# Optimization experiments

Hardware: AMD Instinct MI355X
Metric: run time of the kernel (lower is better)

The kernel has to match this reference:

```python
import jax, jax.numpy as jnp
import numpy as np

N = 100000       # nodes
E = 3200000      # edges (avg degree 32)
IN_F = 256
OUT_F = 128


def setup_inputs() -> dict:
    key = jax.random.key(0)
    k1, k2, k3, k4, k5, k6 = jax.random.split(key, 6)
    x = jax.random.normal(k1, (N, IN_F), dtype=jnp.float32)
    adj_row = jax.random.randint(k2, (E,), 0, N, dtype=jnp.int64)
    adj_col = jax.random.randint(k3, (E,), 0, N, dtype=jnp.int64)
    adj_val = jax.random.uniform(k4, (E,), dtype=jnp.float32)
    stdv = 1.0 / np.sqrt(OUT_F)
    weight = jax.random.uniform(k5, (IN_F, OUT_F), dtype=jnp.float32, minval=-stdv, maxval=stdv)
    bias = jax.random.uniform(k6, (OUT_F,), dtype=jnp.float32, minval=-stdv, maxval=stdv)
    return {"x": x, "adj_row": adj_row, "adj_col": adj_col,
            "adj_val": adj_val, "weight": weight, "bias": bias}


def reference(x, adj_row, adj_col, adj_val, weight, bias):
    # dropout with p=0 is identity
    support = x @ weight                                   # [N, OUT_F] dense GEMM
    # spmm(adj, support): gather neighbor rows, scale by edge value, segment-sum into rows
    gathered = adj_val[:, None] * support[adj_col]         # [E, OUT_F]
    out = jax.ops.segment_sum(gathered, adj_row, num_segments=N)  # [N, OUT_F]
    return jax.nn.relu(out + bias)
```

## Files before the change

kernel.cpp:

```cpp
#include <hip/hip_runtime.h>

#define N_NODES 100000
#define IN_F 256
#define OUT_F 128
#define RPB 64
#define RSHIFT 6
#define NB 1563
#define CAPG 2560
#define CHUNK_SC 4096

typedef short bf16x8 __attribute__((ext_vector_type(8)));
typedef float f32x4  __attribute__((ext_vector_type(4)));

static __device__ __forceinline__ unsigned short f2bf(float f) {
    unsigned int u = __float_as_uint(f);
    u = (u + 0x7FFF + ((u >> 16) & 1)) >> 16;
    return (unsigned short)u;
}

__global__ __launch_bounds__(256) void wt_kernel(const float* __restrict__ w,
                                                 unsigned short* __restrict__ wT,
                                                 int* __restrict__ gcur) {
    int n = blockIdx.x;
    int k = threadIdx.x;
    wT[n * IN_F + k] = f2bf(w[(size_t)k * OUT_F + n]);
    if (blockIdx.x < 7) {
        int i = blockIdx.x * 256 + threadIdx.x;
        if (i < NB) gcur[i] = i * CAPG;
    }
}

__global__ __launch_bounds__(256) void gemm_mfma_kernel(const float* __restrict__ x,
                                                        const unsigned short* __restrict__ wT,
                                                        unsigned short* __restrict__ supb) {
    __shared__ unsigned short A_lds[32][264];

    const int tid  = threadIdx.x;
    const int wave = tid >> 6;
    const int lane = tid & 63;
    const int quad = lane >> 4;
    const int l15  = lane & 15;
    const int row_base = blockIdx.x * 32;

    bf16x8 bfrag[2][8];
    {
        const unsigned short* wb = wT + (size_t)(wave * 32 + l15) * IN_F + quad * 8;
#pragma unroll
        for (int ct = 0; ct < 2; ++ct)
#pragma unroll
            for (int ks = 0; ks < 8; ++ks)
                bfrag[ct][ks] = *(const bf16x8*)(wb + ct * 16 * IN_F + ks * 32);
    }

    {
        const float* xb = x + (size_t)row_base * IN_F;
#pragma unroll
        for (int i = 0; i < 8; ++i) {
            int fidx = i * 1024 + tid * 4;
            float4 a = *(const float4*)(xb + fidx);
            int r = fidx >> 8;
            int c = fidx & 255;
            ushort4 u = {f2bf(a.x), f2bf(a.y), f2bf(a.z), f2bf(a.w)};
            *(ushort4*)&A_lds[r][c] = u;
        }
    }
    __syncthreads();

    f32x4 acc[2][2];
#pragma unroll
    for (int rt = 0; rt < 2; ++rt)
#pragma unroll
        for (int ct = 0; ct < 2; ++ct) acc[rt][ct] = (f32x4){0.f, 0.f, 0.f, 0.f};

#pragma unroll
    for (int ks = 0; ks < 8; ++ks) {
        bf16x8 a0 = *(const bf16x8*)&A_lds[l15][ks * 32 + quad * 8];
        bf16x8 a1 = *(const bf16x8*)&A_lds[16 + l15][ks * 32 + quad * 8];
        acc[0][0] = __builtin_amdgcn_mfma_f32_16x16x32_bf16(a0, bfrag[0][ks], acc[0][0], 0, 0, 0);
        acc[0][1] = __builtin_amdgcn_mfma_f32_16x16x32_bf16(a0, bfrag[1][ks], acc[0][1], 0, 0, 0);
        acc[1][0] = __builtin_amdgcn_mfma_f32_16x16x32_bf16(a1, bfrag[0][ks], acc[1][0], 0, 0, 0);
        acc[1][1] = __builtin_amdgcn_mfma_f32_16x16x32_bf16(a1, bfrag[1][ks], acc[1][1], 0, 0, 0);
    }

#pragma unroll
    for (int rt = 0; rt < 2; ++rt)
#pragma unroll
        for (int ct = 0; ct < 2; ++ct)
#pragma unroll
            for (int r = 0; r < 4; ++r) {
                int orow = row_base + rt * 16 + quad * 4 + r;
                int ocol = wave * 32 + ct * 16 + l15;
                supb[(size_t)orow * OUT_F + ocol] = f2bf(acc[rt][ct][r]);
            }
}

__global__ __launch_bounds__(256) void scatter_kernel(const int* __restrict__ adj_row,
                                                      const int* __restrict__ adj_col,
                                                      const float* __restrict__ adj_val,
                                                      int* __restrict__ gcur,
                                                      int2* __restrict__ ebuf, int E) {
    __shared__ int pref[NB + 1];
    __shared__ int shf[NB];
    __shared__ int2 se[CHUNK_SC];
    __shared__ int wsum[4];

    const int tid  = threadIdx.x;
    const int base = blockIdx.x * CHUNK_SC;
    const int m    = min(CHUNK_SC, E - base);
    const int nv   = m >> 2;

    for (int b = tid; b <= NB; b += 256) pref[b] = 0;
    __syncthreads();

    for (int j = tid; j < nv; j += 256) {
        int4 r4 = ((const int4*)(adj_row + base))[j];
        atomicAdd(&pref[r4.x >> RSHIFT], 1);
        atomicAdd(&pref[r4.y >> RSHIFT], 1);
        atomicAdd(&pref[r4.z >> RSHIFT], 1);
        atomicAdd(&pref[r4.w >> RSHIFT], 1);
    }
    if (tid < (m & 3)) atomicAdd(&pref[adj_row[base + (nv << 2) + tid] >> RSHIFT], 1);
    __syncthreads();

    {
        int loc[7];
        const int bb = tid * 7;
        int s = 0;
#pragma unroll
        for (int g = 0; g < 7; ++g) {
            int b = bb + g;
            int v = (b < NB) ? pref[b] : 0;
            loc[g] = s;
            s += v;
        }
        const int lane = tid & 63, wv = tid >> 6;
        int inc = s;
        for (int d = 1; d < 64; d <<= 1) {
            int t = __shfl_up(inc, d, 64);
            if (lane >= d) inc += t;
        }
        if (lane == 63) wsum[wv] = inc;
        __syncthreads();
        int wb2 = 0;
        for (int k = 0; k < wv; ++k) wb2 += wsum[k];
        const int texcl = wb2 + inc - s;
#pragma unroll
        for (int g = 0; g < 7; ++g) {
            int b = bb + g;
            if (b < NB) pref[b] = texcl + loc[g];
        }
        if (tid == 255) pref[NB] = texcl + s;
    }
    __syncthreads();

    for (int b = tid; b < NB; b += 256) {
        int s0 = pref[b];
        int c  = pref[b + 1] - s0;
        if (c > 0) shf[b] = atomicAdd(&gcur[b], c) - s0;
    }
    __syncthreads();

    for (int j = tid; j < nv; j += 256) {
        int4   c4 = ((const int4*)(adj_col + base))[j];
        int4   r4 = ((const int4*)(adj_row + base))[j];
        float4 v4 = ((const float4*)(adj_val + base))[j];
        int p;
        p = atomicAdd(&pref[r4.x >> RSHIFT], 1);
        se[p] = make_int2(c4.x | ((r4.x & (RPB - 1)) << 17), __float_as_int(v4.x));
        p = atomicAdd(&pref[r4.y >> RSHIFT], 1);
        se[p] = make_int2(c4.y | ((r4.y & (RPB - 1)) << 17), __float_as_int(v4.y));
        p = atomicAdd(&pref[r4.z >> RSHIFT], 1);
        se[p] = make_int2(c4.z | ((r4.z & (RPB - 1)) << 17), __float_as_int(v4.z));
        p = atomicAdd(&pref[r4.w >> RSHIFT], 1);
        se[p] = make_int2(c4.w | ((r4.w & (RPB - 1)) << 17), __float_as_int(v4.w));
    }
    if (tid < (m & 3)) {
        int i = base + (nv << 2) + tid;
        int r = adj_row[i];
        int p = atomicAdd(&pref[r >> RSHIFT], 1);
        se[p] = make_int2(adj_col[i] | ((r & (RPB - 1)) << 17), __float_as_int(adj_val[i]));
    }
    __syncthreads();

    for (int p = tid; p < m; p += 256) {
        int lo = 0, hi = NB - 1;
        while (lo < hi) {
            int mid = (lo + hi) >> 1;
            if (pref[mid] > p) hi = mid; else lo = mid + 1;
        }
        int g = shf[lo] + p;
        if (g < (lo + 1) * CAPG) ebuf[g] = se[p];
    }
}

__global__ __launch_bounds__(512) void spmm_kernel(const int2* __restrict__ ebuf,
                                                   const int* __restrict__ gcur,
                                                   const unsigned short* __restrict__ supb,
                                                   const float* __restrict__ bias,
                                                   float* __restrict__ out) {
    __shared__ int2 se[CAPG];
    __shared__ int cnt[RPB];
    __shared__ int off[RPB];
    __shared__ int cur[RPB];

    const int tid  = threadIdx.x;
    const int b    = blockIdx.x;
    const int wave = tid >> 6;
    const int lane = tid & 63;
    const int f0   = lane * 2;

    const int start = b * CAPG;
    int m = gcur[b] - start;
    if (m > CAPG) m = CAPG;

    if (tid < RPB) cnt[tid] = 0;
    __syncthreads();

    int2 ev[5];
#pragma unroll
    for (int j = 0; j < 5; ++j) {
        int i = j * 512 + tid;
        if (i < m) {
            ev[j] = ebuf[start + i];
            atomicAdd(&cnt[ev[j].x >> 17], 1);
        }
    }
    __syncthreads();

    if (tid < RPB) {
        int v = cnt[tid];
        int s = v;
#pragma unroll
        for (int d = 1; d < RPB; d <<= 1) {
            int t = __shfl_up(s, d, 64);
            if (tid >= d) s += t;
        }
        off[tid] = s - v;
        cur[tid] = s - v;
    }
    __syncthreads();

#pragma unroll
    for (int j = 0; j < 5; ++j) {
        int i = j * 512 + tid;
        if (i < m) {
            int p = atomicAdd(&cur[ev[j].x >> 17], 1);
            se[p] = ev[j];
        }
    }
    __syncthreads();

    float2 acc[8];
#pragma unroll
    for (int j = 0; j < 8; ++j) acc[j] = make_float2(0.f, 0.f);

#pragma unroll
    for (int j = 0; j < 8; ++j) {
        int r = wave * 8 + j;
        int o = off[r];
        int c = cnt[r];
        float2 a = acc[j];
        int i = 0;
        for (; i + 4 <= c; i += 4) {
            int2 e0 = se[o + i + 0];
            int2 e1 = se[o + i + 1];
            int2 e2 = se[o + i + 2];
            int2 e3 = se[o + i + 3];
            unsigned int u0 = *(const unsigned int*)(supb + (size_t)(e0.x & 0x1FFFF) * OUT_F + f0);
            unsigned int u1 = *(const unsigned int*)(supb + (size_t)(e1.x & 0x1FFFF) * OUT_F + f0);
            unsigned int u2 = *(const unsigned int*)(supb + (size_t)(e2.x & 0x1FFFF) * OUT_F + f0);
            unsigned int u3 = *(const unsigned int*)(supb + (size_t)(e3.x & 0x1FFFF) * OUT_F + f0);
            float v0 = __int_as_float(e0.y), v1 = __int_as_float(e1.y);
            float v2 = __int_as_float(e2.y), v3 = __int_as_float(e3.y);
            a.x += v0 * __uint_as_float(u0 << 16);
            a.y += v0 * __uint_as_float(u0 & 0xFFFF0000u);
            a.x += v1 * __uint_as_float(u1 << 16);
            a.y += v1 * __uint_as_float(u1 & 0xFFFF0000u);
            a.x += v2 * __uint_as_float(u2 << 16);
            a.y += v2 * __uint_as_float(u2 & 0xFFFF0000u);
            a.x += v3 * __uint_as_float(u3 << 16);
            a.y += v3 * __uint_as_float(u3 & 0xFFFF0000u);
        }
        for (; i < c; ++i) {
            int2 e = se[o + i];
            unsigned int u = *(const unsigned int*)(supb + (size_t)(e.x & 0x1FFFF) * OUT_F + f0);
            float v = __int_as_float(e.y);
            a.x += v * __uint_as_float(u << 16);
            a.y += v * __uint_as_float(u & 0xFFFF0000u);
        }
        acc[j] = a;
    }

    float2 bv = *((const float2*)bias + lane);
    const int rbase = b << RSHIFT;
#pragma unroll
    for (int j = 0; j < 8; ++j) {
        int grow = rbase + wave * 8 + j;
        if (grow < N_NODES) {
            float2 o;
            o.x = fmaxf(acc[j].x + bv.x, 0.f);
            o.y = fmaxf(acc[j].y + bv.y, 0.f);
            *((float2*)(out + (size_t)grow * OUT_F) + lane) = o;
        }
    }
}

extern "C" void kernel_launch(void* const* d_in, const int* in_sizes, int n_in,
                              void* d_out, int out_size, void* d_ws, size_t ws_size,
                              hipStream_t stream) {
    const float* x       = (const float*)d_in[0];
    const int*   adj_row = (const int*)d_in[1];
    const int*   adj_col = (const int*)d_in[2];
    const float* adj_val = (const float*)d_in[3];
    const float* weight  = (const float*)d_in[4];
    const float* bias    = (const float*)d_in[5];
    float* out = (float*)d_out;
    const int E = in_sizes[1];

    char* p = (char*)d_ws;
    unsigned short* supb = (unsigned short*)p;  p += (size_t)N_NODES * OUT_F * 2;
    int2* ebuf           = (int2*)p;            p += (size_t)NB * CAPG * 8;
    unsigned short* wT   = (unsigned short*)p;  p += (size_t)OUT_F * IN_F * 2;
    int* gcur            = (int*)p;             p += (size_t)NB * 4;

    wt_kernel<<<OUT_F, 256, 0, stream>>>(weight, wT, gcur);
    gemm_mfma_kernel<<<N_NODES / 32, 256, 0, stream>>>(x, wT, supb);
    scatter_kernel<<<(E + CHUNK_SC - 1) / CHUNK_SC, 256, 0, stream>>>(adj_row, adj_col,
                                                                      adj_val, gcur, ebuf, E);
    spmm_kernel<<<NB, 512, 0, stream>>>(ebuf, gcur, supb, bias, out);
}
```

Baseline: 372.0 us.

## Replace bucketed LDS edge sort with global per-row CSR built via atomics

Drops the two-level bucketed scatter (per-chunk LDS sort into fixed-capacity 64-row groups, then a per-block LDS re-sort in spmm). Instead it builds an exact CSR: row degree histogram fused into the GEMM kernel with global atomics, a three-kernel prefix scan, a global-atomic scatter into per-row slots, and an spmm that reads each row's edges straight from global memory. This removes the LDS re-sort and the capacity-truncation risk. In exchange it adds millions of contended global atomics, uncoalesced scattered 8-byte writes, and three extra kernel launches plus a memset.

```diff
diff --git a/kernel.cpp b/kernel.cpp
--- a/kernel.cpp
+++ b/kernel.cpp
@@ -3,11 +3,7 @@
 #define N_NODES 100000
 #define IN_F 256
 #define OUT_F 128
-#define RPB 64
-#define RSHIFT 6
-#define NB 1563
-#define CAPG 2560
-#define CHUNK_SC 4096
+#define ROWS_PER_SBLK 391
 
 typedef short bf16x8 __attribute__((ext_vector_type(8)));
 typedef float f32x4  __attribute__((ext_vector_type(4)));
@@ -19,20 +15,17 @@
 }
 
 __global__ __launch_bounds__(256) void wt_kernel(const float* __restrict__ w,
-                                                 unsigned short* __restrict__ wT,
-                                                 int* __restrict__ gcur) {
+                                                 unsigned short* __restrict__ wT) {
     int n = blockIdx.x;
     int k = threadIdx.x;
     wT[n * IN_F + k] = f2bf(w[(size_t)k * OUT_F + n]);
-    if (blockIdx.x < 7) {
-        int i = blockIdx.x * 256 + threadIdx.x;
-        if (i < NB) gcur[i] = i * CAPG;
-    }
 }
 
 __global__ __launch_bounds__(256) void gemm_mfma_kernel(const float* __restrict__ x,
                                                         const unsigned short* __restrict__ wT,
-                                                        unsigned short* __restrict__ supb) {
+                                                        unsigned short* __restrict__ supb,
+                                                        const int* __restrict__ adj_row,
+                                                        int* __restrict__ rowcnt, int E) {
     __shared__ unsigned short A_lds[32][264];
 
     const int tid  = threadIdx.x;
@@ -41,6 +34,19 @@
     const int quad = lane >> 4;
     const int l15  = lane & 15;
     const int row_base = blockIdx.x * 32;
+
+    {
+        const int nv4 = E >> 2;
+        for (int i = blockIdx.x * 256 + tid; i < nv4; i += 3125 * 256) {
+            int4 r4 = ((const int4*)adj_row)[i];
+            atomicAdd(&rowcnt[r4.x], 1);
+            atomicAdd(&rowcnt[r4.y], 1);
+            atomicAdd(&rowcnt[r4.z], 1);
+            atomicAdd(&rowcnt[r4.w], 1);
+        }
+        if (blockIdx.x == 0 && tid < (E & 3))
+            atomicAdd(&rowcnt[adj_row[(nv4 << 2) + tid]], 1);
+    }
 
     bf16x8 bfrag[2][8];
     {
@@ -94,182 +100,124 @@
             }
 }
 
+__global__ __launch_bounds__(256) void scan1_kernel(const int* __restrict__ rowcnt,
+                                                    int* __restrict__ bsum) {
+    __shared__ int ws[4];
+    const int g = blockIdx.x, tid = threadIdx.x;
+    const int base = g * ROWS_PER_SBLK;
+    int s = 0;
+    for (int i = tid; i < ROWS_PER_SBLK; i += 256) {
+        int r = base + i;
+        if (r < N_NODES) s += rowcnt[r];
+    }
+#pragma unroll
+    for (int d = 1; d < 64; d <<= 1) s += __shfl_xor(s, d, 64);
+    if ((tid & 63) == 0) ws[tid >> 6] = s;
+    __syncthreads();
+    if (tid == 0) bsum[g] = ws[0] + ws[1] + ws[2] + ws[3];
+}
+
+__global__ __launch_bounds__(256) void scan2_kernel(const int* __restrict__ bsum,
+                                                    int* __restrict__ bbase) {
+    __shared__ int ws[4];
+    const int tid = threadIdx.x;
+    const int lane = tid & 63, wv = tid >> 6;
+    int v = bsum[tid];
+    int inc = v;
+#pragma unroll
+    for (int d = 1; d < 64; d <<= 1) {
+        int t = __shfl_up(inc, d, 64);
+        if (lane >= d) inc += t;
+    }
+    if (lane == 63) ws[wv] = inc;
+    __syncthreads();
+    int wb = 0;
+    for (int k = 0; k < wv; ++k) wb += ws[k];
+    bbase[tid] = wb + inc - v;
+}
+
+__global__ __launch_bounds__(256) void scan3_kernel(const int* __restrict__ rowcnt,
+                                                    const int* __restrict__ bbase,
+                                                    int* __restrict__ rowoff,
+                                                    int* __restrict__ rowcur) {
+    __shared__ int ws[4];
+    const int g = blockIdx.x, tid = threadIdx.x;
+    const int base = g * ROWS_PER_SBLK;
+    const int r0 = base + 2 * tid, r1 = r0 + 1;
+    const bool ok0 = (2 * tid < ROWS_PER_SBLK) && (r0 < N_NODES);
+    const bool ok1 = (2 * tid + 1 < ROWS_PER_SBLK) && (r1 < N_NODES);
+    int a = ok0 ? rowcnt[r0] : 0;
+    int b = ok1 ? rowcnt[r1] : 0;
+    int s = a + b;
+    const int lane = tid & 63, wv = tid >> 6;
+    int inc = s;
+#pragma unroll
+    for (int d = 1; d < 64; d <<= 1) {
+        int t = __shfl_up(inc, d, 64);
+        if (lane >= d) inc += t;
+    }
+    if (lane == 63) ws[wv] = inc;
+    __syncthreads();
+    int wb = 0;
+    for (int k = 0; k < wv; ++k) wb += ws[k];
+    const int excl = bbase[g] + wb + inc - s;
+    if (ok0) { rowoff[r0] = excl;     rowcur[r0] = excl; }
+    if (ok1) { rowoff[r1] = excl + a; rowcur[r1] = excl + a; }
+}
+
 __global__ __launch_bounds__(256) void scatter_kernel(const int* __restrict__ adj_row,
                                                       const int* __restrict__ adj_col,
                                                       const float* __restrict__ adj_val,
-                                                      int* __restrict__ gcur,
+                                                      int* __restrict__ rowcur,
                                                       int2* __restrict__ ebuf, int E) {
-    __shared__ int pref[NB + 1];
-    __shared__ int shf[NB];
-    __shared__ int2 se[CHUNK_SC];
-    __shared__ int wsum[4];
-
-    const int tid  = threadIdx.x;
-    const int base = blockIdx.x * CHUNK_SC;
-    const int m    = min(CHUNK_SC, E - base);
-    const int nv   = m >> 2;
-
-    for (int b = tid; b <= NB; b += 256) pref[b] = 0;
-    __syncthreads();
-
-    for (int j = tid; j < nv; j += 256) {
-        int4 r4 = ((const int4*)(adj_row + base))[j];
-        atomicAdd(&pref[r4.x >> RSHIFT], 1);
-        atomicAdd(&pref[r4.y >> RSHIFT], 1);
-        atomicAdd(&pref[r4.z >> RSHIFT], 1);
-        atomicAdd(&pref[r4.w >> RSHIFT], 1);
-    }
-    if (tid < (m & 3)) atomicAdd(&pref[adj_row[base + (nv << 2) + tid] >> RSHIFT], 1);
-    __syncthreads();
-
-    {
-        int loc[7];
-        const int bb = tid * 7;
-        int s = 0;
-#pragma unroll
-        for (int g = 0; g < 7; ++g) {
-            int b = bb + g;
-            int v = (b < NB) ? pref[b] : 0;
-            loc[g] = s;
-            s += v;
-        }
-        const int lane = tid & 63, wv = tid >> 6;
-        int inc = s;
-        for (int d = 1; d < 64; d <<= 1) {
-            int t = __shfl_up(inc, d, 64);
-            if (lane >= d) inc += t;
-        }
-        if (lane == 63) wsum[wv] = inc;
-        __syncthreads();
-        int wb2 = 0;
-        for (int k = 0; k < wv; ++k) wb2 += wsum[k];
-        const int texcl = wb2 + inc - s;
-#pragma unroll
-        for (int g = 0; g < 7; ++g) {
-            int b = bb + g;
-            if (b < NB) pref[b] = texcl + loc[g];
-        }
-        if (tid == 255) pref[NB] = texcl + s;
-    }
-    __syncthreads();
-
-    for (int b = tid; b < NB; b += 256) {
-        int s0 = pref[b];
-        int c  = pref[b + 1] - s0;
-        if (c > 0) shf[b] = atomicAdd(&gcur[b], c) - s0;
-    }
-    __syncthreads();
-
-    for (int j = tid; j < nv; j += 256) {
-        int4   c4 = ((const int4*)(adj_col + base))[j];
-        int4   r4 = ((const int4*)(adj_row + base))[j];
-        float4 v4 = ((const float4*)(adj_val + base))[j];
+    const int gid = blockIdx.x * 256 + threadIdx.x;
+    const int nv4 = E >> 2;
+    for (int j = gid; j < nv4; j += gridDim.x * 256) {
+        int4   r4 = ((const int4*)adj_row)[j];
+        int4   c4 = ((const int4*)adj_col)[j];
+        float4 v4 = ((const float4*)adj_val)[j];
         int p;
-        p = atomicAdd(&pref[r4.x >> RSHIFT], 1);
-        se[p] = make_int2(c4.x | ((r4.x & (RPB - 1)) << 17), __float_as_int(v4.x));
-        p = atomicAdd(&pref[r4.y >> RSHIFT], 1);
-        se[p] = make_int2(c4.y | ((r4.y & (RPB - 1)) << 17), __float_as_int(v4.y));
-        p = atomicAdd(&pref[r4.z >> RSHIFT], 1);
-        se[p] = make_int2(c4.z | ((r4.z & (RPB - 1)) << 17), __float_as_int(v4.z));
-        p = atomicAdd(&pref[r4.w >> RSHIFT], 1);
-        se[p] = make_int2(c4.w | ((r4.w & (RPB - 1)) << 17), __float_as_int(v4.w));
-    }
-    if (tid < (m & 3)) {
-        int i = base + (nv << 2) + tid;
-        int r = adj_row[i];
-        int p = atomicAdd(&pref[r >> RSHIFT], 1);
-        se[p] = make_int2(adj_col[i] | ((r & (RPB - 1)) << 17), __float_as_int(adj_val[i]));
-    }
-    __syncthreads();
-
-    for (int p = tid; p < m; p += 256) {
-        int lo = 0, hi = NB - 1;
-        while (lo < hi) {
-            int mid = (lo + hi) >> 1;
-            if (pref[mid] > p) hi = mid; else lo = mid + 1;
-        }
-        int g = shf[lo] + p;
-        if (g < (lo + 1) * CAPG) ebuf[g] = se[p];
-    }
-}
-
-__global__ __launch_bounds__(512) void spmm_kernel(const int2* __restrict__ ebuf,
-                                                   const int* __restrict__ gcur,
+        p = atomicAdd(&rowcur[r4.x], 1); ebuf[p] = make_int2(c4.x, __float_as_int(v4.x));
+        p = atomicAdd(&rowcur[r4.y], 1); ebuf[p] = make_int2(c4.y, __float_as_int(v4.y));
+        p = atomicAdd(&rowcur[r4.z], 1); ebuf[p] = make_int2(c4.z, __float_as_int(v4.z));
+        p = atomicAdd(&rowcur[r4.w], 1); ebuf[p] = make_int2(c4.w, __float_as_int(v4.w));
+    }
+    if (gid < (E & 3)) {
+        int i = (nv4 << 2) + gid;
+        int p = atomicAdd(&rowcur[adj_row[i]], 1);
+        ebuf[p] = make_int2(adj_col[i], __float_as_int(adj_val[i]));
+    }
+}
+
+__global__ __launch_bounds__(256) void spmm_kernel(const int2* __restrict__ ebuf,
+                                                   const int* __restrict__ rowoff,
+                                                   const int* __restrict__ rowend,
                                                    const unsigned short* __restrict__ supb,
                                                    const float* __restrict__ bias,
                                                    float* __restrict__ out) {
-    __shared__ int2 se[CAPG];
-    __shared__ int cnt[RPB];
-    __shared__ int off[RPB];
-    __shared__ int cur[RPB];
-
     const int tid  = threadIdx.x;
-    const int b    = blockIdx.x;
-    const int wave = tid >> 6;
+    const int wave = __builtin_amdgcn_readfirstlane(tid >> 6);
     const int lane = tid & 63;
     const int f0   = lane * 2;
-
-    const int start = b * CAPG;
-    int m = gcur[b] - start;
-    if (m > CAPG) m = CAPG;
-
-    if (tid < RPB) cnt[tid] = 0;
-    __syncthreads();
-
-    int2 ev[5];
-#pragma unroll
-    for (int j = 0; j < 5; ++j) {
-        int i = j * 512 + tid;
-        if (i < m) {
-            ev[j] = ebuf[start + i];
-            atomicAdd(&cnt[ev[j].x >> 17], 1);
-        }
-    }
-    __syncthreads();
-
-    if (tid < RPB) {
-        int v = cnt[tid];
-        int s = v;
-#pragma unroll
-        for (int d = 1; d < RPB; d <<= 1) {
-            int t = __shfl_up(s, d, 64);
-            if (tid >= d) s += t;
-        }
-        off[tid] = s - v;
-        cur[tid] = s - v;
-    }
-    __syncthreads();
-
-#pragma unroll
-    for (int j = 0; j < 5; ++j) {
-        int i = j * 512 + tid;
-        if (i < m) {
-            int p = atomicAdd(&cur[ev[j].x >> 17], 1);
-            se[p] = ev[j];
-        }
-    }
-    __syncthreads();
-
-    float2 acc[8];
-#pragma unroll
-    for (int j = 0; j < 8; ++j) acc[j] = make_float2(0.f, 0.f);
-
-#pragma unroll
+    const int rbase = blockIdx.x * 32 + wave * 8;
+    const float2 bv = *((const float2*)bias + lane);
+
     for (int j = 0; j < 8; ++j) {
-        int r = wave * 8 + j;
-        int o = off[r];
-        int c = cnt[r];
-        float2 a = acc[j];
+        const int r = rbase + j;
+        const int o = rowoff[r];
+        const int c = rowend[r] - o;
+        const int2* ep = ebuf + o;
+        float2 a = make_float2(0.f, 0.f);
         int i = 0;
         for (; i + 4 <= c; i += 4) {
-            int2 e0 = se[o + i + 0];
-            int2 e1 = se[o + i + 1];
-            int2 e2 = se[o + i + 2];
-            int2 e3 = se[o + i + 3];
-            unsigned int u0 = *(const unsigned int*)(supb + (size_t)(e0.x & 0x1FFFF) * OUT_F + f0);
-            unsigned int u1 = *(const unsigned int*)(supb + (size_t)(e1.x & 0x1FFFF) * OUT_F + f0);
-            unsigned int u2 = *(const unsigned int*)(supb + (size_t)(e2.x & 0x1FFFF) * OUT_F + f0);
-            unsigned int u3 = *(const unsigned int*)(supb + (size_t)(e3.x & 0x1FFFF) * OUT_F + f0);
+            int2 e0 = ep[i + 0];
+            int2 e1 = ep[i + 1];
+            int2 e2 = ep[i + 2];
+            int2 e3 = ep[i + 3];
+            unsigned int u0 = *(const unsigned int*)(supb + (size_t)e0.x * OUT_F + f0);
+            unsigned int u1 = *(const unsigned int*)(supb + (size_t)e1.x * OUT_F + f0);
+            unsigned int u2 = *(const unsigned int*)(supb + (size_t)e2.x * OUT_F + f0);
+            unsigned int u3 = *(const unsigned int*)(supb + (size_t)e3.x * OUT_F + f0);
             float v0 = __int_as_float(e0.y), v1 = __int_as_float(e1.y);
             float v2 = __int_as_float(e2.y), v3 = __int_as_float(e3.y);
             a.x += v0 * __uint_as_float(u0 << 16);
@@ -282,26 +230,16 @@
             a.y += v3 * __uint_as_float(u3 & 0xFFFF0000u);
         }
         for (; i < c; ++i) {
-            int2 e = se[o + i];
-            unsigned int u = *(const unsigned int*)(supb + (size_t)(e.x & 0x1FFFF) * OUT_F + f0);
+            int2 e = ep[i];
+            unsigned int u = *(const unsigned int*)(supb + (size_t)e.x * OUT_F + f0);
             float v = __int_as_float(e.y);
             a.x += v * __uint_as_float(u << 16);
             a.y += v * __uint_as_float(u & 0xFFFF0000u);
         }
-        acc[j] = a;
-    }
-
-    float2 bv = *((const float2*)bias + lane);
-    const int rbase = b << RSHIFT;
-#pragma unroll
-    for (int j = 0; j < 8; ++j) {
-        int grow = rbase + wave * 8 + j;
-        if (grow < N_NODES) {
-            float2 o;
-            o.x = fmaxf(acc[j].x + bv.x, 0.f);
-            o.y = fmaxf(acc[j].y + bv.y, 0.f);
-            *((float2*)(out + (size_t)grow * OUT_F) + lane) = o;
-        }
+        float2 ov;
+        ov.x = fmaxf(a.x + bv.x, 0.f);
+        ov.y = fmaxf(a.y + bv.y, 0.f);
+        *((float2*)(out + (size_t)r * OUT_F) + lane) = ov;
     }
 }
 
@@ -319,13 +257,20 @@
 
     char* p = (char*)d_ws;
     unsigned short* supb = (unsigned short*)p;  p += (size_t)N_NODES * OUT_F * 2;
-    int2* ebuf           = (int2*)p;            p += (size_t)NB * CAPG * 8;
+    int2* ebuf           = (int2*)p;            p += (size_t)E * 8;
     unsigned short* wT   = (unsigned short*)p;  p += (size_t)OUT_F * IN_F * 2;
-    int* gcur            = (int*)p;             p += (size_t)NB * 4;
-
-    wt_kernel<<<OUT_F, 256, 0, stream>>>(weight, wT, gcur);
-    gemm_mfma_kernel<<<N_NODES / 32, 256, 0, stream>>>(x, wT, supb);
-    scatter_kernel<<<(E + CHUNK_SC - 1) / CHUNK_SC, 256, 0, stream>>>(adj_row, adj_col,
-                                                                      adj_val, gcur, ebuf, E);
-    spmm_kernel<<<NB, 512, 0, stream>>>(ebuf, gcur, supb, bias, out);
-}
+    int* rowcnt          = (int*)p;             p += (size_t)N_NODES * 4;
+    int* rowoff          = (int*)p;             p += (size_t)N_NODES * 4;
+    int* rowcur          = (int*)p;             p += (size_t)N_NODES * 4;
+    int* bsum            = (int*)p;             p += 256 * 4;
+    int* bbase           = (int*)p;             p += 256 * 4;
+
+    hipMemsetAsync(rowcnt, 0, (size_t)N_NODES * 4, stream);
+    wt_kernel<<<OUT_F, 256, 0, stream>>>(weight, wT);
+    gemm_mfma_kernel<<<N_NODES / 32, 256, 0, stream>>>(x, wT, supb, adj_row, rowcnt, E);
+    scan1_kernel<<<256, 256, 0, stream>>>(rowcnt, bsum);
+    scan2_kernel<<<1, 256, 0, stream>>>(bsum, bbase);
+    scan3_kernel<<<256, 256, 0, stream>>>(rowcnt, bbase, rowoff, rowcur);
+    scatter_kernel<<<2048, 256, 0, stream>>>(adj_row, adj_col, adj_val, rowcur, ebuf, E);
+    spmm_kernel<<<N_NODES / 32, 256, 0, stream>>>(ebuf, rowoff, rowcur, supb, bias, out);
+}
```

Result: slower. 636.0 us (+71.0%).
